# Kernel tuning notes

Hardware: AMD Instinct MI355X
Metric: run time of the kernel (lower is better)

The kernel has to match this reference:

```python
import jax, jax.numpy as jnp
import numpy as np

B, N, M = 2, 4096, 12288
K, SH, H, GK, NC, F = 64, 32, 64, 8, 200, 1


def sph_to_cart(theta, phi):
    st = jnp.sin(theta)
    return jnp.stack([st * jnp.cos(phi), st * jnp.sin(phi), jnp.cos(theta)], axis=-1)


def setup_inputs() -> dict:
    key = jax.random.key(0)
    ks = jax.random.split(key, 16)
    theta = jax.random.uniform(ks[0], (B, N)) * jnp.pi
    phi = jax.random.uniform(ks[1], (B, N)) * 2 * jnp.pi
    feat = jax.random.normal(ks[2], (B, N))
    xxx = jnp.stack([theta, phi, feat], axis=1)  # [B,3,N]
    pt = jax.random.uniform(ks[3], (M,)) * jnp.pi
    pp = jax.random.uniform(ks[4], (M,)) * 2 * jnp.pi
    pix_theta_phi = jnp.stack([pt, pp], axis=1)  # [M,2]
    s = 0.1
    return dict(
        xxx=xxx,
        pix_theta_phi=pix_theta_phi,
        att_w1=jax.random.normal(ks[5], (F + 1, SH)) * s,
        att_b1=jnp.zeros((SH,)),
        att_w2=jax.random.normal(ks[6], (SH, 1)) * s,
        att_b2=jnp.zeros((1,)),
        proj_w=jax.random.normal(ks[7], (F, H)) * s,
        proj_b=jnp.zeros((H,)),
        rel_w=jax.random.normal(ks[8], (3, H, H)) * s,
        rel_b=jnp.zeros((3, H)),
        root_w=jax.random.normal(ks[9], (3, H, H)) * s,
        out_w1=jax.random.normal(ks[10], (H, H)) * s,
        out_b1=jnp.zeros((H,)),
        out_w2=jax.random.normal(ks[11], (H, NC)) * s,
        out_b2=jnp.zeros((NC,)),
    )


def reference(xxx, pix_theta_phi, att_w1, att_b1, att_w2, att_b2, proj_w, proj_b,
              rel_w, rel_b, root_w, out_w1, out_b1, out_w2, out_b2):
    # --- sparse healpix sampler ---
    los_tp = jnp.transpose(xxx[:, :2, :], (0, 2, 1))   # [B,N,2]
    x = xxx[:, 2, :][..., None]                        # [B,N,1]
    r_los = sph_to_cart(los_tp[..., 0], los_tp[..., 1])           # [B,N,3]
    r_pix = sph_to_cart(pix_theta_phi[:, 0], pix_theta_phi[:, 1])  # [M,3]
    cos = jnp.clip(jnp.einsum('bnc,mc->bmn', r_los, r_pix), -1.0, 1.0)  # [B,M,N]
    vals, idx = jax.lax.top_k(cos, K)                  # [B,M,K]
    x_g = jax.vmap(lambda xb, ib: xb[ib])(x, idx)      # [B,M,K,F]
    d = jnp.arccos(jnp.clip(vals, -1.0, 1.0))          # [B,M,K]
    feat = jnp.concatenate([x_g, d[..., None]], axis=-1)  # [B,M,K,F+1]
    logits = jax.nn.relu(feat @ att_w1 + att_b1) @ att_w2 + att_b2  # [B,M,K,1]
    w = jax.nn.softmax(logits[..., 0], axis=-1)        # [B,M,K]
    pooled = jnp.einsum('bmk,bmkf->bmf', w, x_g)       # [B,M,F]
    # --- GNN on healpix grid ---
    h = jax.nn.relu(pooled @ proj_w + proj_b)          # [B,M,H]
    m = r_pix.shape[0]
    sq = jnp.sum(r_pix * r_pix, axis=1)
    d2 = sq[:, None] + sq[None, :] - 2.0 * (r_pix @ r_pix.T)       # [M,M]
    d2 = jnp.where(jnp.eye(m, dtype=bool), jnp.inf, d2)  # loop=False
    _, nbr = jax.lax.top_k(-d2, GK)                    # [M,GK] knn_graph
    for i in range(rel_w.shape[0]):
        agg = h[:, nbr, :].sum(axis=2)                 # sum-aggregate neighbor msgs
        h = jax.nn.relu(agg @ rel_w[i] + rel_b[i] + h @ root_w[i])
    graph_feat = h.mean(axis=1)                        # global_mean_pool -> [B,H]
    out = jax.nn.relu(graph_feat @ out_w1 + out_b1) @ out_w2 + out_b2
    return out
```

## Files before the change

### kernel.cpp

```cpp
#include <hip/hip_runtime.h>
#include <hip/hip_bf16.h>

#define B_ 2
#define N_ 4096
#define M_ 12288
#define K_ 64
#define SH_ 32
#define H_ 64
#define GK_ 8
#define NC_ 200

#define KCAP 128
#define BCAP2 48
#define SCAP 192
#define MG_ 0.01f
#define C256_ 81.48733086f

static __device__ __forceinline__ unsigned f2key(float f) {
  unsigned b = __float_as_uint(f);
  return (b & 0x80000000u) ? ~b : (b | 0x80000000u);
}
static __device__ __forceinline__ float key2f(unsigned u) {
  unsigned b = (u & 0x80000000u) ? (u & 0x7fffffffu) : ~u;
  return __uint_as_float(b);
}
static __device__ __forceinline__ unsigned long long shflxor64(unsigned long long x, int m) {
  unsigned lo = (unsigned)x, hi = (unsigned)(x >> 32);
  lo = (unsigned)__shfl_xor((int)lo, m);
  hi = (unsigned)__shfl_xor((int)hi, m);
  return ((unsigned long long)hi << 32) | lo;
}
static __device__ __forceinline__ unsigned long long kpack(float s, int j) {
  return ((unsigned long long)f2key(s) << 14) | (unsigned)(16383 - j);
}
static __device__ __forceinline__ unsigned long long spack(float c, int n) {
  return ((unsigned long long)f2key(c) << 12) | (unsigned)(4095 - n);
}
static __device__ __forceinline__ int thbkt(float th) {
  int b = (int)(th * C256_);
  return b < 0 ? 0 : (b > 255 ? 255 : b);
}
static __device__ __forceinline__ float clamp1(float x) { return fminf(1.f, fmaxf(-1.f, x)); }
static __device__ __forceinline__ float rdlane(float v, int c) {
  return __uint_as_float((unsigned)__builtin_amdgcn_readlane((int)__float_as_uint(v), c));
}

__global__ __launch_bounds__(256) void sentinel_vF(float* out, int n, float val) {
  int t = blockIdx.x * 256 + threadIdx.x;
  if (t < n) out[t] = val;
}

#define GRIDB_ 129
#define PREPN_ (M_ + B_*N_ + B_*H_)
#define PREPB_ ((PREPN_ + 255)/256)

__global__ __launch_bounds__(256) void prep_vF(
    const float* __restrict__ xxx, const float* __restrict__ pix,
    float4* __restrict__ r_pix, float4* __restrict__ r_los, float* __restrict__ gf,
    float* __restrict__ kthrG, float* __restrict__ cthrG, unsigned* __restrict__ cnt)
{
  const float PI = 3.14159265358979f;
  if ((int)blockIdx.x < GRIDB_) {
    int gid  = blockIdx.x*4 + (threadIdx.x >> 6);
    if (gid >= 514) return;
    int lane = threadIdx.x & 63;
    int tgt  = (gid >= 257) ? 1 : 0;
    int gp   = gid - tgt*257;
    float thp = (float)gp * (PI/256.f);
    float cp = cosf(thp), sp = fmaxf(sinf(thp), 1e-6f);
    float thq = ((float)lane + 0.5f) * (PI/64.f);
    float sq = sinf(thq), cq = cosf(thq);
    float rinv = 1.0f / (sq * sp);
    float At = tgt ? (2.f*PI*PI*128.f/(float)N_) : (2.f*PI*PI*48.f/(float)M_);
    float lo = 1e-3f, hi = 3.1414f;
    for (int it = 0; it < 12; ++it) {
      float al = 0.5f*(lo + hi);
      float ca = cosf(al);
      float arg = clamp1((ca - cq*cp) * rinv);
      float ax = fabsf(arg);
      float ac = sqrtf(fmaxf(0.f, 1.f - ax)) *
                 fmaf(ax, fmaf(ax, fmaf(ax, -0.0187293f, 0.0742610f), -0.2121144f), 1.5707288f);
      ac = (arg < 0.f) ? (PI - ac) : ac;
      float S = ac;
      #pragma unroll
      for (int off = 32; off; off >>= 1) S += __shfl_xor(S, off);
      float A = 2.f * S * (PI/64.f);
      if (A < At) lo = al; else hi = al;
    }
    if (lane == 0) {
      float chv = cosf(hi);
      if (tgt) cthrG[gp] = chv - 1e-5f;
      else     kthrG[gp] = 2.f*chv - 1.00002f;
    }
  } else {
    int tid = ((int)blockIdx.x - GRIDB_)*256 + threadIdx.x;
    if (tid < M_) {
      float th = pix[2*tid], ph = pix[2*tid+1];
      float st = sinf(th);
      float x = st*cosf(ph), y = st*sinf(ph), z = cosf(th);
      r_pix[tid] = make_float4(x, y, z, x*x + y*y + z*z);
      atomicAdd(&cnt[thbkt(th)], 1u);
    }
    int t2 = tid - M_;
    if (t2 >= 0 && t2 < B_*N_) {
      int b = t2 >> 12, n = t2 & (N_-1);
      const float* xb = xxx + b*3*N_;
      float th = xb[n], ph = xb[N_+n], ft = xb[2*N_+n];
      float st = sinf(th);
      r_los[t2] = make_float4(st*cosf(ph), st*sinf(ph), cosf(th), ft);
      atomicAdd(&cnt[256 + b*256 + thbkt(th)], 1u);
    }
    int t3 = tid - M_ - B_*N_;
    if (t3 >= 0 && t3 < B_*H_) gf[t3] = 0.0f;
  }
}

__global__ __launch_bounds__(256) void scan_vF(
    const unsigned* __restrict__ cnt, int* __restrict__ pstart, int* __restrict__ lstart,
    unsigned* __restrict__ pcur, unsigned* __restrict__ lcur)
{
  __shared__ unsigned buf[256];
  const int t = threadIdx.x;
  for (int arr = 0; arr < 3; ++arr) {
    unsigned v = cnt[arr*256 + t];
    buf[t] = v;
    __syncthreads();
    for (int off = 1; off < 256; off <<= 1) {
      unsigned o = (t >= off) ? buf[t - off] : 0u;
      __syncthreads();
      buf[t] += o;
      __syncthreads();
    }
    unsigned incl = buf[t], excl = incl - v;
    if (arr == 0) {
      pstart[t] = (int)excl; if (t == 255) pstart[256] = (int)incl;
      pcur[t] = excl;
    } else {
      int b = arr - 1;
      lstart[b*257 + t] = (int)excl; if (t == 255) lstart[b*257 + 256] = (int)incl;
      lcur[b*256 + t] = excl;
    }
    __syncthreads();
  }
}

__global__ __launch_bounds__(256) void scatter_vF(
    const float* __restrict__ xxx, const float* __restrict__ pix,
    const float4* __restrict__ r_pix, const float4* __restrict__ r_los,
    unsigned* __restrict__ pcur, unsigned* __restrict__ lcur,
    float4* __restrict__ spix, int* __restrict__ sjdx,
    float4* __restrict__ slos, int* __restrict__ sldx)
{
  int tid = blockIdx.x * 256 + threadIdx.x;
  if (tid < M_) {
    int bkt = thbkt(pix[2*tid]);
    unsigned pos = atomicAdd(&pcur[bkt], 1u);
    spix[pos] = r_pix[tid];
    sjdx[pos] = tid;
  } else {
    int t2 = tid - M_;
    if (t2 < B_*N_) {
      int b = t2 >> 12, n = t2 & (N_-1);
      int bkt = thbkt(xxx[b*3*N_ + n]);
      unsigned pos = atomicAdd(&lcur[b*256 + bkt], 1u);
      slos[b*N_ + pos] = r_los[t2];
      sldx[b*N_ + pos] = n;
    }
  }
}

__global__ __launch_bounds__(512) void sampler_vF(
    const float* __restrict__ pix,
    const float4* __restrict__ spix, const int* __restrict__ sjdx,
    const float4* __restrict__ slos, const int* __restrict__ sldx,
    const int* __restrict__ lstart, const float4* __restrict__ r_los,
    const float* __restrict__ cthrG,
    const float* __restrict__ aw1, const float* __restrict__ ab1,
    const float* __restrict__ aw2, const float* __restrict__ ab2,
    float* __restrict__ pooled)
{
  __shared__ unsigned long long cand[16][SCAP];
  __shared__ unsigned long long selKey[16][K_];
  __shared__ unsigned long long bndK[16][BCAP2];
  __shared__ unsigned hist[16][64];

  const int tid = threadIdx.x, wv = tid >> 6, lane = tid & 63;
  const int b  = blockIdx.y;
  const int srow0 = blockIdx.x*16 + wv*2, srow1 = srow0 + 1;
  const int r0 = wv*2, r1 = r0 + 1;
  const int m0 = sjdx[srow0], m1 = sjdx[srow1];
  const float4 p0 = spix[srow0], p1 = spix[srow1];
  const float thp0 = pix[2*m0], thp1 = pix[2*m1];
  const int g0 = thbkt(thp0), g1 = thbkt(thp1);
  const float th0 = fminf(cthrG[g0], cthrG[g0+1]);
  const float th1 = fminf(cthrG[g1], cthrG[g1+1]);
  const float inv0 = 63.999f / (1.000001f - th0);
  const float inv1 = 63.999f / (1.000001f - th1);
  const float4* sl = slos + b * N_;
  const int* sx = sldx + b * N_;
  const float4* rl = r_los + b * N_;
  const int* ls = lstart + b * 257;
  const unsigned long long ltm = (1ull << lane) - 1ull;

  int jlo, jhi;
  {
    float al0 = acosf(clamp1(th0)), al1 = acosf(clamp1(th1));
    int blo = thbkt(fminf(thp0 - al0, thp1 - al1) - MG_);
    int bhi = thbkt(fmaxf(thp0 + al0, thp1 + al1) + MG_);
    jlo = ls[blo]; jhi = ls[bhi + 1];
  }

  unsigned cnt0 = 0, cnt1 = 0;
  for (int base = jlo; base < jhi; base += 64) {
    int pos = base + lane;
    bool act = pos < jhi;
    float c0 = -2.f, c1 = -2.f; int n = 0;
    if (act) {
      float4 v = sl[pos]; n = sx[pos];
      c0 = clamp1(v.x*p0.x + v.y*p0.y + v.z*p0.z);
      c1 = clamp1(v.x*p1.x + v.y*p1.y + v.z*p1.z);
    }
    bool pr0 = c0 > th0, pr1 = c1 > th1;
    unsigned long long mk0 = __ballot(pr0);
    if (mk0) {
      unsigned off = (unsigned)__popcll(mk0 & ltm);
      if (pr0 && cnt0 + off < SCAP) cand[r0][cnt0 + off] = spack(c0, n);
      cnt0 += (unsigned)__popcll(mk0);
    }
    unsigned long long mk1 = __ballot(pr1);
    if (mk1) {
      unsigned off = (unsigned)__popcll(mk1 & ltm);
      if (pr1 && cnt1 + off < SCAP) cand[r1][cnt1 + off] = spack(c1, n);
      cnt1 += (unsigned)__popcll(mk1);
    }
  }

  for (int rr = 0; rr < 2; ++rr) {
    const int r = (rr == 0) ? r0 : r1;
    const int m = (rr == 0) ? m0 : m1;
    const float4 p = (rr == 0) ? p0 : p1;
    const float thp = (rr == 0) ? thp0 : thp1;
    const float thg = (rr == 0) ? th0 : th1;
    const float invg = (rr == 0) ? inv0 : inv1;
    unsigned cn = (rr == 0) ? cnt0 : cnt1;
    bool fin = false;

    if (cn >= (unsigned)K_ && cn <= (unsigned)SCAP) {
      hist[r][lane] = 0u;
      for (int i = lane; i < (int)cn; i += 64) {
        float c = key2f((unsigned)(cand[r][i] >> 12));
        atomicAdd(&hist[r][(int)((c - thg) * invg)], 1u);
      }
      unsigned g = hist[r][lane], s = g;
      #pragma unroll
      for (int off = 1; off < 64; off <<= 1) {
        unsigned t2 = (unsigned)__shfl_down((int)s, off);
        s += (lane + off < 64) ? t2 : 0u;
      }
      unsigned snext = s - g;
      unsigned packed = (s >= K_ && snext < K_) ? (((unsigned)(lane+1) << 16) | snext) : 0u;
      #pragma unroll
      for (int off = 32; off; off >>= 1) {
        unsigned o = (unsigned)__shfl_xor((int)packed, off);
        packed = packed > o ? packed : o;
      }
      const int t = (int)(packed >> 16) - 1;
      const unsigned chi = packed & 0xFFFFu;
      const unsigned need = K_ - chi;

      unsigned hiC = 0, bdC = 0;
      for (int i0 = 0; i0 < (int)cn; i0 += 64) {
        int i = i0 + lane;
        bool act = i < (int)cn;
        unsigned long long key = act ? cand[r][i] : 0ull;
        int bin = -1;
        if (act) bin = (int)((key2f((unsigned)(key >> 12)) - thg) * invg);
        bool pHi = act && bin > t, pBd = act && bin == t;
        unsigned long long mH = __ballot(pHi);
        unsigned offH = (unsigned)__popcll(mH & ltm);
        if (pHi && hiC + offH < K_) selKey[r][hiC + offH] = key;
        hiC += (unsigned)__popcll(mH);
        unsigned long long mB = __ballot(pBd);
        unsigned offB = (unsigned)__popcll(mB & ltm);
        if (pBd && bdC + offB < BCAP2) bndK[r][bdC + offB] = key;
        bdC += (unsigned)__popcll(mB);
      }
      if (bdC <= (unsigned)BCAP2) {
        if (lane < (int)bdC) {
          unsigned long long ki = bndK[r][lane];
          int rank = 0;
          for (int j = 0; j < (int)bdC; ++j) rank += (bndK[r][j] > ki) ? 1 : 0;
          if ((unsigned)rank < need) selKey[r][chi + rank] = ki;
        }
        fin = true;
      }
    }

    if (!fin) {
      float th = thg;
      float inv = invg;
      int wlo = jlo, whi = jhi;

      if (cn >= (unsigned)K_) {
        hist[r][lane] = 0u;
        cn = 0;
        for (int base = wlo; base < whi; base += 64) {
          int pos = base + lane;
          bool act = pos < whi;
          float c = -2.f;
          if (act) {
            float4 v = sl[pos];
            c = clamp1(v.x*p.x + v.y*p.y + v.z*p.z);
          }
          bool pr = c > th;
          if (pr) atomicAdd(&hist[r][(int)((c - th) * inv)], 1u);
          cn += (unsigned)__popcll(__ballot(pr));
        }
      }

      int tries = 0;
      while (cn < K_ && tries < 3) {
        th = 1.f - 1.6f*(1.f - th); ++tries;
        inv = 63.999f / (1.000001f - th);
        float al = acosf(clamp1(th));
        int blo = thbkt(thp - al - MG_), bhi = thbkt(thp + al + MG_);
        wlo = ls[blo]; whi = ls[bhi + 1];
        hist[r][lane] = 0u;
        cn = 0;
        for (int base = wlo; base < whi; base += 64) {
          int pos = base + lane;
          bool act = pos < whi;
          float c = -2.f;
          if (act) {
            float4 v = sl[pos];
            c = clamp1(v.x*p.x + v.y*p.y + v.z*p.z);
          }
          bool pr = c > th;
          if (pr) atomicAdd(&hist[r][(int)((c - th) * inv)], 1u);
          cn += (unsigned)__popcll(__ballot(pr));
        }
      }

      bool fin2 = false;
      if (cn >= K_) {
        unsigned g = hist[r][lane], s = g;
        #pragma unroll
        for (int off = 1; off < 64; off <<= 1) {
          unsigned t2 = (unsigned)__shfl_down((int)s, off);
          s += (lane + off < 64) ? t2 : 0u;
        }
        unsigned snext = s - g;
        unsigned packed = (s >= K_ && snext < K_) ? (((unsigned)(lane+1) << 16) | snext) : 0u;
        #pragma unroll
        for (int off = 32; off; off >>= 1) {
          unsigned o = (unsigned)__shfl_xor((int)packed, off);
          packed = packed > o ? packed : o;
        }
        const int t = (int)(packed >> 16) - 1;
        const unsigned chi = packed & 0xFFFFu;
        const unsigned need = K_ - chi;

        unsigned hiC = 0, bdC = 0;
        for (int base = wlo; base < whi; base += 64) {
          int pos = base + lane;
          bool act = pos < whi;
          float c = -2.f; int n = 0;
          if (act) {
            float4 v = sl[pos]; n = sx[pos];
            c = clamp1(v.x*p.x + v.y*p.y + v.z*p.z);
          }
          int bin = (act && c > th) ? (int)((c - th) * inv) : -1;
          bool pHi = bin > t;
          bool pBd = bin == t;
          unsigned long long mH = __ballot(pHi);
          unsigned offH = (unsigned)__popcll(mH & ltm);
          if (pHi && hiC + offH < K_) selKey[r][hiC + offH] = spack(c, n);
          hiC += (unsigned)__popcll(mH);
          unsigned long long mB = __ballot(pBd);
          unsigned offB = (unsigned)__popcll(mB & ltm);
          if (pBd && bdC + offB < BCAP2) bndK[r][bdC + offB] = spack(c, n);
          bdC += (unsigned)__popcll(mB);
        }
        if (bdC <= (unsigned)BCAP2) {
          if (lane < (int)bdC) {
            unsigned long long ki = bndK[r][lane];
            int rank = 0;
            for (int j = 0; j < (int)bdC; ++j) rank += (bndK[r][j] > ki) ? 1 : 0;
            if ((unsigned)rank < need) selKey[r][chi + rank] = ki;
          }
          fin2 = true;
        }
      }

      if (!fin2) {
        unsigned long long prev = ~0ull;
        for (int rd = 0; rd < K_; ++rd) {
          unsigned long long best = 0ull;
          for (int i = 0; i < 64; ++i) {
            int n = lane + 64*i;
            float4 v = rl[n];
            float c = clamp1(v.x*p.x + v.y*p.y + v.z*p.z);
            unsigned long long k = spack(c, n);
            if (k < prev && k > best) best = k;
          }
          #pragma unroll
          for (int off = 1; off < 64; off <<= 1) {
            unsigned long long o = shflxor64(best, off);
            best = o > best ? o : best;
          }
          if (lane == 0) selKey[r][rd] = best;
          prev = best;
        }
      }
    }

    {
      unsigned long long key = selKey[r][lane];
      int n = 4095 - (int)(key & 0xFFFull);
      float c = key2f((unsigned)(key >> 12));
      float xg = rl[n].w;
      float d  = acosf(clamp1(c));
      float acc = ab2[0];
      for (int s2 = 0; s2 < SH_; ++s2)
        acc += fmaxf(xg*aw1[s2] + d*aw1[SH_+s2] + ab1[s2], 0.f) * aw2[s2];
      float mx = acc;
      #pragma unroll
      for (int off = 32; off; off >>= 1) mx = fmaxf(mx, __shfl_xor(mx, off));
      float e = expf(acc - mx);
      float se = e, sxe = e * xg;
      #pragma unroll
      for (int off = 32; off; off >>= 1) { se += __shfl_xor(se, off); sxe += __shfl_xor(sxe, off); }
      if (lane == 0) pooled[b*M_ + m] = sxe / se;
    }
  }
}

__global__ __launch_bounds__(512) void knn_vF(
    const float* __restrict__ pix,
    const float4* __restrict__ spix, const int* __restrict__ sjdx,
    const int* __restrict__ pstart, const float4* __restrict__ r_pix,
    const float* __restrict__ kthrG, int* __restrict__ nbr)
{
  __shared__ unsigned long long cKey[16][KCAP];

  const int tid = threadIdx.x, wv = tid >> 6, lane = tid & 63;
  const int lr0 = wv*2;
  const int srow0 = blockIdx.x*16 + lr0, srow1 = srow0 + 1;
  const int i0 = sjdx[srow0], i1 = sjdx[srow1];
  const float4 p0 = spix[srow0], p1 = spix[srow1];
  const float thp0 = pix[2*i0], thp1 = pix[2*i1];
  const int g0 = thbkt(thp0), g1 = thbkt(thp1);
  const float t0 = fminf(kthrG[g0], kthrG[g0+1]);
  const float t1 = fminf(kthrG[g1], kthrG[g1+1]);
  const unsigned long long ltm = (1ull << lane) - 1ull;

  unsigned cnt0 = 0, cnt1 = 0;
  {
    float al0 = acosf(clamp1((t0 + 1.00002f)*0.5f));
    float al1 = acosf(clamp1((t1 + 1.00002f)*0.5f));
    int blo = thbkt(fminf(thp0 - al0, thp1 - al1) - MG_);
    int bhi = thbkt(fmaxf(thp0 + al0, thp1 + al1) + MG_);
    int jlo = pstart[blo], jhi = pstart[bhi + 1];
    for (int base = jlo; base < jhi; base += 64) {
      int pos = base + lane;
      bool act = pos < jhi;
      float s0 = -1e30f, s1 = -1e30f; int j = -1;
      if (act) {
        float4 v = spix[pos]; j = sjdx[pos];
        s0 = 2.f*(p0.x*v.x + p0.y*v.y + p0.z*v.z) - v.w;
        s1 = 2.f*(p1.x*v.x + p1.y*v.y + p1.z*v.z) - v.w;
      }
      bool pr0 = act && (j != i0) && (s0 > t0);
      bool pr1 = act && (j != i1) && (s1 > t1);
      unsigned long long mk0 = __ballot(pr0);
      if (mk0) {
        unsigned off = (unsigned)__popcll(mk0 & ltm);
        if (pr0 && cnt0 + off < KCAP) cKey[lr0][cnt0 + off] = kpack(s0, j);
        cnt0 += (unsigned)__popcll(mk0);
      }
      unsigned long long mk1 = __ballot(pr1);
      if (mk1) {
        unsigned off = (unsigned)__popcll(mk1 & ltm);
        if (pr1 && cnt1 + off < KCAP) cKey[lr0+1][cnt1 + off] = kpack(s1, j);
        cnt1 += (unsigned)__popcll(mk1);
      }
    }
  }

  for (int rr = 0; rr < 2; ++rr) {
    const int lr = lr0 + rr;
    const int i  = (rr == 0) ? i0 : i1;
    const float4 pi = (rr == 0) ? p0 : p1;
    const float thp = (rr == 0) ? thp0 : thp1;
    float th = (rr == 0) ? t0 : t1;
    unsigned cn = (rr == 0) ? cnt0 : cnt1;

    int tries = 0;
    while (cn < (unsigned)GK_ && tries < 3) {
      th = 1.6f*th - 0.6f; ++tries;
      float al = acosf(clamp1((th + 1.00002f)*0.5f));
      int blo = thbkt(thp - al - MG_), bhi = thbkt(thp + al + MG_);
      int jlo = pstart[blo], jhi = pstart[bhi + 1];
      cn = 0;
      for (int base = jlo; base < jhi; base += 64) {
        int pos = base + lane;
        bool act = pos < jhi;
        float s = -1e30f; int j = -1;
        if (act) {
          float4 v = spix[pos]; j = sjdx[pos];
          s = 2.f*(pi.x*v.x + pi.y*v.y + pi.z*v.z) - v.w;
        }
        bool pr = act && (j != i) && (s > th);
        unsigned long long mk = __ballot(pr);
        if (mk) {
          unsigned off = (unsigned)__popcll(mk & ltm);
          if (pr && cn + off < KCAP) cKey[lr][cn + off] = kpack(s, j);
          cn += (unsigned)__popcll(mk);
        }
      }
    }

    if (cn >= (unsigned)GK_ && cn <= (unsigned)KCAP) {
      unsigned long long pk[2];
      #pragma unroll
      for (int t2 = 0; t2 < 2; ++t2) {
        int idx = lane + 64*t2;
        pk[t2] = (idx < (int)cn) ? cKey[lr][idx] : 0ull;
      }
      for (int round = 0; round < GK_; ++round) {
        unsigned long long loc = pk[0]; int lt = 0;
        if (pk[1] > loc) { loc = pk[1]; lt = 1; }
        unsigned long long best = loc;
        #pragma unroll
        for (int off = 1; off < 64; off <<= 1) {
          unsigned long long o = shflxor64(best, off);
          best = o > best ? o : best;
        }
        if (loc == best) pk[lt] = 0ull;
        if (lane == round) nbr[i*GK_ + round] = 16383 - (int)(best & 16383ull);
      }
    } else {
      unsigned long long prev = ~0ull;
      for (int rd = 0; rd < GK_; ++rd) {
        unsigned long long best = 0ull;
        for (int j = lane; j < M_; j += 64) {
          float4 v = r_pix[j];
          float s = 2.f*(pi.x*v.x + pi.y*v.y + pi.z*v.z) - v.w;
          if (j != i) {
            unsigned long long k = kpack(s, j);
            if (k < prev && k > best) best = k;
          }
        }
        #pragma unroll
        for (int off = 1; off < 64; off <<= 1) {
          unsigned long long o = shflxor64(best, off);
          best = o > best ? o : best;
        }
        if (lane == rd) nbr[i*GK_ + rd] = 16383 - (int)(best & 16383ull);
        prev = best;
      }
    }
  }
}

__global__ __launch_bounds__(256) void gnn1f_vF(
    const float* __restrict__ pooled, float* __restrict__ hout, const int* __restrict__ nbr,
    const float* __restrict__ pw, const float* __restrict__ pb,
    const float* __restrict__ relw, const float* __restrict__ relb,
    const float* __restrict__ rootw)
{
  __shared__ float wrel[H_*H_], wroot[H_*H_];
  const int tid = threadIdx.x;
  #pragma unroll
  for (int q = 0; q < 16; ++q) {
    int idx = tid + 256*q;
    wrel[idx]  = relw[idx];
    wroot[idx] = rootw[idx];
  }
  __syncthreads();

  const int lane = tid & 63;
  const int wave = tid >> 6;
  const int b = blockIdx.y;
  const int m0 = blockIdx.x * 16 + wave * 4;
  const float* pldb = pooled + (size_t)b * M_;
  const float pwl = pw[lane], pbl = pb[lane], rbl = relb[lane];

  float h[4], agg[4], acc[4];
  #pragma unroll
  for (int t = 0; t < 4; ++t) {
    int m = m0 + t;
    float ps = pldb[m];
    h[t] = fmaxf(ps*pwl + pbl, 0.f);
    float a = 0.f;
    #pragma unroll
    for (int k = 0; k < GK_; ++k) {
      int nb = nbr[m*GK_ + k];
      nb = nb < 0 ? 0 : (nb >= M_ ? M_-1 : nb);
      float pn = pldb[nb];
      a += fmaxf(pn*pwl + pbl, 0.f);
    }
    agg[t] = a;
    acc[t] = rbl;
  }
  #pragma unroll
  for (int c = 0; c < H_; ++c) {
    float wr = wrel[c*H_ + lane], wo = wroot[c*H_ + lane];
    #pragma unroll
    for (int t = 0; t < 4; ++t)
      acc[t] += rdlane(agg[t], c) * wr + rdlane(h[t], c) * wo;
  }
  #pragma unroll
  for (int t = 0; t < 4; ++t)
    hout[((size_t)b*M_ + m0 + t)*H_ + lane] = fmaxf(acc[t], 0.f);
}

__global__ __launch_bounds__(256) void gnn_vF(
    const float* __restrict__ hin, float* __restrict__ hout, const int* __restrict__ nbr,
    const float* __restrict__ relw, const float* __restrict__ relb,
    const float* __restrict__ rootw)
{
  __shared__ float wrel[H_*H_], wroot[H_*H_];
  const int tid = threadIdx.x;
  #pragma unroll
  for (int q = 0; q < 16; ++q) {
    int idx = tid + 256*q;
    wrel[idx]  = relw[idx];
    wroot[idx] = rootw[idx];
  }
  __syncthreads();

  const int lane = tid & 63;
  const int wave = tid >> 6;
  const int b = blockIdx.y;
  const int m0 = blockIdx.x * 16 + wave * 4;
  const float* hb = hin + (size_t)b * M_ * H_;
  const float rbl = relb[lane];

  float h[4], agg[4], acc[4];
  #pragma unroll
  for (int t = 0; t < 4; ++t) {
    int m = m0 + t;
    h[t] = hb[m*H_ + lane];
    float a = 0.f;
    #pragma unroll
    for (int k = 0; k < GK_; ++k) {
      int nb = nbr[m*GK_ + k];
      nb = nb < 0 ? 0 : (nb >= M_ ? M_-1 : nb);
      a += hb[nb*H_ + lane];
    }
    agg[t] = a;
    acc[t] = rbl;
  }
  #pragma unroll
  for (int c = 0; c < H_; ++c) {
    float wr = wrel[c*H_ + lane], wo = wroot[c*H_ + lane];
    #pragma unroll
    for (int t = 0; t < 4; ++t)
      acc[t] += rdlane(agg[t], c) * wr + rdlane(h[t], c) * wo;
  }
  #pragma unroll
  for (int t = 0; t < 4; ++t)
    hout[((size_t)b*M_ + m0 + t)*H_ + lane] = fmaxf(acc[t], 0.f);
}

__global__ __launch_bounds__(256) void gnn3r_vF(
    const float* __restrict__ hin, float* __restrict__ gf, const int* __restrict__ nbr,
    const float* __restrict__ relw, const float* __restrict__ relb,
    const float* __restrict__ rootw)
{
  __shared__ float wrel[H_*H_], wroot[H_*H_];
  __shared__ float gacc[H_];
  const int tid = threadIdx.x;
  #pragma unroll
  for (int q = 0; q < 16; ++q) {
    int idx = tid + 256*q;
    wrel[idx]  = relw[idx];
    wroot[idx] = rootw[idx];
  }
  if (tid < H_) gacc[tid] = 0.f;
  __syncthreads();

  const int lane = tid & 63;
  const int wave = tid >> 6;
  const int b = blockIdx.y;
  const int m0 = blockIdx.x * 16 + wave * 4;
  const float* hb = hin + (size_t)b * M_ * H_;
  const float rbl = relb[lane];

  float h[4], agg[4], acc[4];
  #pragma unroll
  for (int t = 0; t < 4; ++t) {
    int m = m0 + t;
    h[t] = hb[m*H_ + lane];
    float a = 0.f;
    #pragma unroll
    for (int k = 0; k < GK_; ++k) {
      int nb = nbr[m*GK_ + k];
      nb = nb < 0 ? 0 : (nb >= M_ ? M_-1 : nb);
      a += hb[nb*H_ + lane];
    }
    agg[t] = a;
    acc[t] = rbl;
  }
  #pragma unroll
  for (int c = 0; c < H_; ++c) {
    float wr = wrel[c*H_ + lane], wo = wroot[c*H_ + lane];
    #pragma unroll
    for (int t = 0; t < 4; ++t)
      acc[t] += rdlane(agg[t], c) * wr + rdlane(h[t], c) * wo;
  }
  float ps = fmaxf(acc[0], 0.f) + fmaxf(acc[1], 0.f) + fmaxf(acc[2], 0.f) + fmaxf(acc[3], 0.f);
  atomicAdd(&gacc[lane], ps);
  __syncthreads();
  if (tid < H_) atomicAdd(&gf[b*H_ + tid], gacc[tid]);
}

__global__ __launch_bounds__(256) void head_vF(
    const float* __restrict__ gf, const float* __restrict__ w1,
    const float* __restrict__ b1, const float* __restrict__ w2,
    const float* __restrict__ b2, float* __restrict__ out)
{
  __shared__ float gfm[B_][H_], hid[B_][H_];
  const int tid = threadIdx.x;
  if (tid < B_*H_) gfm[tid >> 6][tid & 63] = gf[tid] * (1.f / (float)M_);
  __syncthreads();
  if (tid < B_*H_) {
    int b = tid >> 6, j = tid & 63;
    float acc = b1[j];
    for (int c = 0; c < H_; ++c) acc += gfm[b][c] * w1[c*H_ + j];
    hid[b][j] = fmaxf(acc, 0.f);
  }
  __syncthreads();
  for (int t = tid; t < B_*NC_; t += 256) {
    int b = t / NC_, o = t - b*NC_;
    float acc = b2[o];
    for (int j = 0; j < H_; ++j) acc += hid[b][j] * w2[j*NC_ + o];
    out[t] = acc;
  }
}

extern "C" void kernel_launch(void* const* d_in, const int* in_sizes, int n_in,
                              void* d_out, int out_size, void* d_ws, size_t ws_size,
                              hipStream_t stream)
{
  float* out = (float*)d_out;

  const size_t need = (size_t)M_*16 + (size_t)B_*N_*16 + (size_t)B_*M_*4
                    + (size_t)M_*GK_*4 + 2*(size_t)B_*M_*H_*4 + (size_t)B_*H_*4;
  bool ok_ws = ws_size >= need;
  bool ok_in = (n_in == 15) && (out_size == B_*NC_)
            && in_sizes[0] == B_*3*N_ && in_sizes[1] == M_*2
            && in_sizes[2] == 2*SH_ && in_sizes[5] == 1
            && in_sizes[8] == 3*H_*H_ && in_sizes[13] == H_*NC_;
  if (!ok_ws || !ok_in) {
    sentinel_vF<<<(out_size + 255)/256, 256, 0, stream>>>(out, out_size, ok_in ? 42.f : 43.f);
    return;
  }

  const float* xxx    = (const float*)d_in[0];
  const float* pix    = (const float*)d_in[1];
  const float* att_w1 = (const float*)d_in[2];
  const float* att_b1 = (const float*)d_in[3];
  const float* att_w2 = (const float*)d_in[4];
  const float* att_b2 = (const float*)d_in[5];
  const float* proj_w = (const float*)d_in[6];
  const float* proj_b = (const float*)d_in[7];
  const float* rel_w  = (const float*)d_in[8];
  const float* rel_b  = (const float*)d_in[9];
  const float* root_w = (const float*)d_in[10];
  const float* out_w1 = (const float*)d_in[11];
  const float* out_b1 = (const float*)d_in[12];
  const float* out_w2 = (const float*)d_in[13];
  const float* out_b2 = (const float*)d_in[14];

  char* w = (char*)d_ws;
  float4* r_pix = (float4*)w;  w += (size_t)M_ * 16;
  float4* r_los = (float4*)w;  w += (size_t)B_ * N_ * 16;
  float*  pooled = (float*)w;  w += (size_t)B_ * M_ * 4;
  int*    nbr = (int*)w;       w += (size_t)M_ * GK_ * 4;
  float*  h0 = (float*)w;      w += (size_t)B_ * M_ * H_ * 4;
  float*  h1 = (float*)w;      w += (size_t)B_ * M_ * H_ * 4;
  float*  gf = (float*)w;      w += (size_t)B_ * H_ * 4;

  float*  kthrG = h0;
  float*  cthrG = h0 + 512;
  float4* spix = (float4*)(h0 + 2*M_);
  int*    sjdx = (int*)(h0 + 6*M_);
  float4* slos = (float4*)(h0 + 7*M_);
  int*    sldx = (int*)(h0 + 7*M_ + 4*B_*N_);
  unsigned* cnt = (unsigned*)(h0 + 7*M_ + 5*B_*N_);
  int*    pstart = (int*)(cnt + 768);
  int*    lstart = pstart + 257;
  unsigned* pcur = (unsigned*)(lstart + 514);
  unsigned* lcur = pcur + 256;

  hipMemsetAsync(cnt, 0, 768*sizeof(unsigned), stream);
  prep_vF<<<GRIDB_ + PREPB_, 256, 0, stream>>>(xxx, pix, r_pix, r_los, gf, kthrG, cthrG, cnt);
  scan_vF<<<1, 256, 0, stream>>>(cnt, pstart, lstart, pcur, lcur);
  scatter_vF<<<(M_ + B_*N_ + 255)/256, 256, 0, stream>>>(xxx, pix, r_pix, r_los, pcur, lcur,
                                                         spix, sjdx, slos, sldx);
  sampler_vF<<<dim3(M_/16, B_), 512, 0, stream>>>(pix, spix, sjdx, slos, sldx, lstart, r_los,
                                                  cthrG, att_w1, att_b1, att_w2, att_b2, pooled);
  knn_vF<<<M_/16, 512, 0, stream>>>(pix, spix, sjdx, pstart, r_pix, kthrG, nbr);
  gnn1f_vF<<<dim3(M_/16, B_), 256, 0, stream>>>(pooled, h1, nbr, proj_w, proj_b,
                                                rel_w + 0*H_*H_, rel_b + 0*H_, root_w + 0*H_*H_);
  gnn_vF<<<dim3(M_/16, B_), 256, 0, stream>>>(h1, h0, nbr, rel_w + 1*H_*H_, rel_b + 1*H_, root_w + 1*H_*H_);
  gnn3r_vF<<<dim3(M_/16, B_), 256, 0, stream>>>(h0, gf, nbr, rel_w + 2*H_*H_, rel_b + 2*H_, root_w + 2*H_*H_);
  head_vF<<<1, 256, 0, stream>>>(gf, out_w1, out_b1, out_w2, out_b2, out);
}
```

Before: 239.2 us.

## Process four query rows per wave in sampler and kNN, tighten candidate thresholds

The sampler and kNN kernels now have each wavefront handle four sorted pixel rows instead of two. Each loaded line-of-sight or pixel vector is reused across four dot products, and the grid is halved. The angular threshold targets are lowered (96 instead of 128 candidates, 40 instead of 48) and the candidate buffer is shrunk to 128, so fewer candidates are gathered and more shared memory fits. The trade-offs are a wider per-wave window, since the union of four rows' ranges is scanned, and a higher chance of falling into the slow fallback paths when fewer than K candidates pass.

Result: slower. 267.6 us (+11.9%).

```diff
diff --git a/kernel.cpp b/kernel.cpp
--- a/kernel.cpp
+++ b/kernel.cpp
@@ -12,7 +12,7 @@
 
 #define KCAP 128
 #define BCAP2 48
-#define SCAP 192
+#define SCAP 128
 #define MG_ 0.01f
 #define C256_ 81.48733086f
 
@@ -45,7 +45,7 @@
   return __uint_as_float((unsigned)__builtin_amdgcn_readlane((int)__float_as_uint(v), c));
 }
 
-__global__ __launch_bounds__(256) void sentinel_vF(float* out, int n, float val) {
+__global__ __launch_bounds__(256) void sentinel_vI(float* out, int n, float val) {
   int t = blockIdx.x * 256 + threadIdx.x;
   if (t < n) out[t] = val;
 }
@@ -54,7 +54,7 @@
 #define PREPN_ (M_ + B_*N_ + B_*H_)
 #define PREPB_ ((PREPN_ + 255)/256)
 
-__global__ __launch_bounds__(256) void prep_vF(
+__global__ __launch_bounds__(256) void prep_vI(
     const float* __restrict__ xxx, const float* __restrict__ pix,
     float4* __restrict__ r_pix, float4* __restrict__ r_los, float* __restrict__ gf,
     float* __restrict__ kthrG, float* __restrict__ cthrG, unsigned* __restrict__ cnt)
@@ -71,7 +71,7 @@
     float thq = ((float)lane + 0.5f) * (PI/64.f);
     float sq = sinf(thq), cq = cosf(thq);
     float rinv = 1.0f / (sq * sp);
-    float At = tgt ? (2.f*PI*PI*128.f/(float)N_) : (2.f*PI*PI*48.f/(float)M_);
+    float At = tgt ? (2.f*PI*PI*96.f/(float)N_) : (2.f*PI*PI*40.f/(float)M_);
     float lo = 1e-3f, hi = 3.1414f;
     for (int it = 0; it < 12; ++it) {
       float al = 0.5f*(lo + hi);
@@ -115,7 +115,7 @@
   }
 }
 
-__global__ __launch_bounds__(256) void scan_vF(
+__global__ __launch_bounds__(256) void scan_vI(
     const unsigned* __restrict__ cnt, int* __restrict__ pstart, int* __restrict__ lstart,
     unsigned* __restrict__ pcur, unsigned* __restrict__ lcur)
 {
@@ -144,7 +144,7 @@
   }
 }
 
-__global__ __launch_bounds__(256) void scatter_vF(
+__global__ __launch_bounds__(256) void scatter_vI(
     const float* __restrict__ xxx, const float* __restrict__ pix,
     const float4* __restrict__ r_pix, const float4* __restrict__ r_los,
     unsigned* __restrict__ pcur, unsigned* __restrict__ lcur,
@@ -169,7 +169,7 @@
   }
 }
 
-__global__ __launch_bounds__(512) void sampler_vF(
+__global__ __launch_bounds__(512) void sampler_vI(
     const float* __restrict__ pix,
     const float4* __restrict__ spix, const int* __restrict__ sjdx,
     const float4* __restrict__ slos, const int* __restrict__ sldx,
@@ -179,79 +179,83 @@
     const float* __restrict__ aw2, const float* __restrict__ ab2,
     float* __restrict__ pooled)
 {
-  __shared__ unsigned long long cand[16][SCAP];
-  __shared__ unsigned long long selKey[16][K_];
-  __shared__ unsigned long long bndK[16][BCAP2];
-  __shared__ unsigned hist[16][64];
+  __shared__ unsigned long long cand[32][SCAP];
+  __shared__ unsigned long long selKey[32][K_];
+  __shared__ unsigned long long bndK[8][BCAP2];
+  __shared__ unsigned hist[8][64];
 
   const int tid = threadIdx.x, wv = tid >> 6, lane = tid & 63;
   const int b  = blockIdx.y;
-  const int srow0 = blockIdx.x*16 + wv*2, srow1 = srow0 + 1;
-  const int r0 = wv*2, r1 = r0 + 1;
-  const int m0 = sjdx[srow0], m1 = sjdx[srow1];
-  const float4 p0 = spix[srow0], p1 = spix[srow1];
-  const float thp0 = pix[2*m0], thp1 = pix[2*m1];
-  const int g0 = thbkt(thp0), g1 = thbkt(thp1);
-  const float th0 = fminf(cthrG[g0], cthrG[g0+1]);
-  const float th1 = fminf(cthrG[g1], cthrG[g1+1]);
-  const float inv0 = 63.999f / (1.000001f - th0);
-  const float inv1 = 63.999f / (1.000001f - th1);
+  const int srow0 = blockIdx.x*32 + wv*4;
+  const int r0 = wv*4;
   const float4* sl = slos + b * N_;
   const int* sx = sldx + b * N_;
   const float4* rl = r_los + b * N_;
   const int* ls = lstart + b * 257;
   const unsigned long long ltm = (1ull << lane) - 1ull;
 
+  float4 p[4]; float thp[4], thr[4], invr[4]; int mI[4];
+  #pragma unroll
+  for (int rr = 0; rr < 4; ++rr) {
+    int sr = srow0 + rr;
+    mI[rr] = sjdx[sr];
+    p[rr] = spix[sr];
+    thp[rr] = pix[2*mI[rr]];
+    int g = thbkt(thp[rr]);
+    thr[rr] = fminf(cthrG[g], cthrG[g+1]);
+    invr[rr] = 63.999f / (1.000001f - thr[rr]);
+  }
+
   int jlo, jhi;
   {
-    float al0 = acosf(clamp1(th0)), al1 = acosf(clamp1(th1));
-    int blo = thbkt(fminf(thp0 - al0, thp1 - al1) - MG_);
-    int bhi = thbkt(fmaxf(thp0 + al0, thp1 + al1) + MG_);
-    jlo = ls[blo]; jhi = ls[bhi + 1];
-  }
-
-  unsigned cnt0 = 0, cnt1 = 0;
+    float wl = 1e9f, wh = -1e9f;
+    #pragma unroll
+    for (int rr = 0; rr < 4; ++rr) {
+      float al = acosf(clamp1(thr[rr]));
+      wl = fminf(wl, thp[rr] - al);
+      wh = fmaxf(wh, thp[rr] + al);
+    }
+    jlo = ls[thbkt(wl - MG_)];
+    jhi = ls[thbkt(wh + MG_) + 1];
+  }
+
+  unsigned cnt[4] = {0u, 0u, 0u, 0u};
   for (int base = jlo; base < jhi; base += 64) {
     int pos = base + lane;
     bool act = pos < jhi;
-    float c0 = -2.f, c1 = -2.f; int n = 0;
-    if (act) {
-      float4 v = sl[pos]; n = sx[pos];
-      c0 = clamp1(v.x*p0.x + v.y*p0.y + v.z*p0.z);
-      c1 = clamp1(v.x*p1.x + v.y*p1.y + v.z*p1.z);
-    }
-    bool pr0 = c0 > th0, pr1 = c1 > th1;
-    unsigned long long mk0 = __ballot(pr0);
-    if (mk0) {
-      unsigned off = (unsigned)__popcll(mk0 & ltm);
-      if (pr0 && cnt0 + off < SCAP) cand[r0][cnt0 + off] = spack(c0, n);
-      cnt0 += (unsigned)__popcll(mk0);
-    }
-    unsigned long long mk1 = __ballot(pr1);
-    if (mk1) {
-      unsigned off = (unsigned)__popcll(mk1 & ltm);
-      if (pr1 && cnt1 + off < SCAP) cand[r1][cnt1 + off] = spack(c1, n);
-      cnt1 += (unsigned)__popcll(mk1);
-    }
-  }
-
-  for (int rr = 0; rr < 2; ++rr) {
-    const int r = (rr == 0) ? r0 : r1;
-    const int m = (rr == 0) ? m0 : m1;
-    const float4 p = (rr == 0) ? p0 : p1;
-    const float thp = (rr == 0) ? thp0 : thp1;
-    const float thg = (rr == 0) ? th0 : th1;
-    const float invg = (rr == 0) ? inv0 : inv1;
-    unsigned cn = (rr == 0) ? cnt0 : cnt1;
+    float4 v = make_float4(0.f, 0.f, 0.f, 0.f); int n = 0;
+    if (act) { v = sl[pos]; n = sx[pos]; }
+    #pragma unroll
+    for (int rr = 0; rr < 4; ++rr) {
+      float c = clamp1(v.x*p[rr].x + v.y*p[rr].y + v.z*p[rr].z);
+      bool pr = act && (c > thr[rr]);
+      unsigned long long mk = __ballot(pr);
+      if (mk) {
+        unsigned off = (unsigned)__popcll(mk & ltm);
+        if (pr && cnt[rr] + off < SCAP) cand[r0+rr][cnt[rr] + off] = spack(c, n);
+        cnt[rr] += (unsigned)__popcll(mk);
+      }
+    }
+  }
+
+  #pragma unroll
+  for (int rr = 0; rr < 4; ++rr) {
+    const int r = r0 + rr;
+    const int m = mI[rr];
+    const float4 pq = p[rr];
+    const float thpq = thp[rr];
+    const float thg = thr[rr];
+    const float invg = invr[rr];
+    unsigned cn = cnt[rr];
     bool fin = false;
 
     if (cn >= (unsigned)K_ && cn <= (unsigned)SCAP) {
-      hist[r][lane] = 0u;
+      hist[wv][lane] = 0u;
       for (int i = lane; i < (int)cn; i += 64) {
         float c = key2f((unsigned)(cand[r][i] >> 12));
-        atomicAdd(&hist[r][(int)((c - thg) * invg)], 1u);
-      }
-      unsigned g = hist[r][lane], s = g;
+        atomicAdd(&hist[wv][(int)((c - thg) * invg)], 1u);
+      }
+      unsigned g = hist[wv][lane], s = g;
       #pragma unroll
       for (int off = 1; off < 64; off <<= 1) {
         unsigned t2 = (unsigned)__shfl_down((int)s, off);
@@ -282,14 +286,14 @@
         hiC += (unsigned)__popcll(mH);
         unsigned long long mB = __ballot(pBd);
         unsigned offB = (unsigned)__popcll(mB & ltm);
-        if (pBd && bdC + offB < BCAP2) bndK[r][bdC + offB] = key;
+        if (pBd && bdC + offB < BCAP2) bndK[wv][bdC + offB] = key;
         bdC += (unsigned)__popcll(mB);
       }
       if (bdC <= (unsigned)BCAP2) {
         if (lane < (int)bdC) {
-          unsigned long long ki = bndK[r][lane];
+          unsigned long long ki = bndK[wv][lane];
           int rank = 0;
-          for (int j = 0; j < (int)bdC; ++j) rank += (bndK[r][j] > ki) ? 1 : 0;
+          for (int j = 0; j < (int)bdC; ++j) rank += (bndK[wv][j] > ki) ? 1 : 0;
           if ((unsigned)rank < need) selKey[r][chi + rank] = ki;
         }
         fin = true;
@@ -302,7 +306,7 @@
       int wlo = jlo, whi = jhi;
 
       if (cn >= (unsigned)K_) {
-        hist[r][lane] = 0u;
+        hist[wv][lane] = 0u;
         cn = 0;
         for (int base = wlo; base < whi; base += 64) {
           int pos = base + lane;
@@ -310,10 +314,10 @@
           float c = -2.f;
           if (act) {
             float4 v = sl[pos];
-            c = clamp1(v.x*p.x + v.y*p.y + v.z*p.z);
+            c = clamp1(v.x*pq.x + v.y*pq.y + v.z*pq.z);
           }
           bool pr = c > th;
-          if (pr) atomicAdd(&hist[r][(int)((c - th) * inv)], 1u);
+          if (pr) atomicAdd(&hist[wv][(int)((c - th) * inv)], 1u);
           cn += (unsigned)__popcll(__ballot(pr));
         }
       }
@@ -323,9 +327,9 @@
         th = 1.f - 1.6f*(1.f - th); ++tries;
         inv = 63.999f / (1.000001f - th);
         float al = acosf(clamp1(th));
-        int blo = thbkt(thp - al - MG_), bhi = thbkt(thp + al + MG_);
+        int blo = thbkt(thpq - al - MG_), bhi = thbkt(thpq + al + MG_);
         wlo = ls[blo]; whi = ls[bhi + 1];
-        hist[r][lane] = 0u;
+        hist[wv][lane] = 0u;
         cn = 0;
         for (int base = wlo; base < whi; base += 64) {
           int pos = base + lane;
@@ -333,17 +337,17 @@
           float c = -2.f;
           if (act) {
             float4 v = sl[pos];
-            c = clamp1(v.x*p.x + v.y*p.y + v.z*p.z);
+            c = clamp1(v.x*pq.x + v.y*pq.y + v.z*pq.z);
           }
           bool pr = c > th;
-          if (pr) atomicAdd(&hist[r][(int)((c - th) * inv)], 1u);
+          if (pr) atomicAdd(&hist[wv][(int)((c - th) * inv)], 1u);
           cn += (unsigned)__popcll(__ballot(pr));
         }
       }
 
       bool fin2 = false;
       if (cn >= K_) {
-        unsigned g = hist[r][lane], s = g;
+        unsigned g = hist[wv][lane], s = g;
         #pragma unroll
         for (int off = 1; off < 64; off <<= 1) {
           unsigned t2 = (unsigned)__shfl_down((int)s, off);
@@ -367,7 +371,7 @@
           float c = -2.f; int n = 0;
           if (act) {
             float4 v = sl[pos]; n = sx[pos];
-            c = clamp1(v.x*p.x + v.y*p.y + v.z*p.z);
+            c = clamp1(v.x*pq.x + v.y*pq.y + v.z*pq.z);
           }
           int bin = (act && c > th) ? (int)((c - th) * inv) : -1;
           bool pHi = bin > t;
@@ -378,14 +382,14 @@
           hiC += (unsigned)__popcll(mH);
           unsigned long long mB = __ballot(pBd);
           unsigned offB = (unsigned)__popcll(mB & ltm);
-          if (pBd && bdC + offB < BCAP2) bndK[r][bdC + offB] = spack(c, n);
+          if (pBd && bdC + offB < BCAP2) bndK[wv][bdC + offB] = spack(c, n);
           bdC += (unsigned)__popcll(mB);
         }
         if (bdC <= (unsigned)BCAP2) {
           if (lane < (int)bdC) {
-            unsigned long long ki = bndK[r][lane];
+            unsigned long long ki = bndK[wv][lane];
             int rank = 0;
-            for (int j = 0; j < (int)bdC; ++j) rank += (bndK[r][j] > ki) ? 1 : 0;
+            for (int j = 0; j < (int)bdC; ++j) rank += (bndK[wv][j] > ki) ? 1 : 0;
             if ((unsigned)rank < need) selKey[r][chi + rank] = ki;
           }
           fin2 = true;
@@ -399,7 +403,7 @@
           for (int i = 0; i < 64; ++i) {
             int n = lane + 64*i;
             float4 v = rl[n];
-            float c = clamp1(v.x*p.x + v.y*p.y + v.z*p.z);
+            float c = clamp1(v.x*pq.x + v.y*pq.y + v.z*pq.z);
             unsigned long long k = spack(c, n);
             if (k < prev && k > best) best = k;
           }
@@ -435,71 +439,73 @@
   }
 }
 
-__global__ __launch_bounds__(512) void knn_vF(
+__global__ __launch_bounds__(512) void knn_vI(
     const float* __restrict__ pix,
     const float4* __restrict__ spix, const int* __restrict__ sjdx,
     const int* __restrict__ pstart, const float4* __restrict__ r_pix,
     const float* __restrict__ kthrG, int* __restrict__ nbr)
 {
-  __shared__ unsigned long long cKey[16][KCAP];
+  __shared__ unsigned long long cKey[32][KCAP];
 
   const int tid = threadIdx.x, wv = tid >> 6, lane = tid & 63;
-  const int lr0 = wv*2;
-  const int srow0 = blockIdx.x*16 + lr0, srow1 = srow0 + 1;
-  const int i0 = sjdx[srow0], i1 = sjdx[srow1];
-  const float4 p0 = spix[srow0], p1 = spix[srow1];
-  const float thp0 = pix[2*i0], thp1 = pix[2*i1];
-  const int g0 = thbkt(thp0), g1 = thbkt(thp1);
-  const float t0 = fminf(kthrG[g0], kthrG[g0+1]);
-  const float t1 = fminf(kthrG[g1], kthrG[g1+1]);
+  const int lr0 = wv*4;
+  const int srow0 = blockIdx.x*32 + lr0;
   const unsigned long long ltm = (1ull << lane) - 1ull;
 
-  unsigned cnt0 = 0, cnt1 = 0;
+  float4 p[4]; float thp[4], thr[4]; int iI[4];
+  #pragma unroll
+  for (int rr = 0; rr < 4; ++rr) {
+    int sr = srow0 + rr;
+    iI[rr] = sjdx[sr];
+    p[rr] = spix[sr];
+    thp[rr] = pix[2*iI[rr]];
+    int g = thbkt(thp[rr]);
+    thr[rr] = fminf(kthrG[g], kthrG[g+1]);
+  }
+
+  unsigned cnt[4] = {0u, 0u, 0u, 0u};
   {
-    float al0 = acosf(clamp1((t0 + 1.00002f)*0.5f));
-    float al1 = acosf(clamp1((t1 + 1.00002f)*0.5f));
-    int blo = thbkt(fminf(thp0 - al0, thp1 - al1) - MG_);
-    int bhi = thbkt(fmaxf(thp0 + al0, thp1 + al1) + MG_);
-    int jlo = pstart[blo], jhi = pstart[bhi + 1];
+    float wl = 1e9f, wh = -1e9f;
+    #pragma unroll
+    for (int rr = 0; rr < 4; ++rr) {
+      float al = acosf(clamp1((thr[rr] + 1.00002f)*0.5f));
+      wl = fminf(wl, thp[rr] - al);
+      wh = fmaxf(wh, thp[rr] + al);
+    }
+    int jlo = pstart[thbkt(wl - MG_)], jhi = pstart[thbkt(wh + MG_) + 1];
     for (int base = jlo; base < jhi; base += 64) {
       int pos = base + lane;
       bool act = pos < jhi;
-      float s0 = -1e30f, s1 = -1e30f; int j = -1;
-      if (act) {
-        float4 v = spix[pos]; j = sjdx[pos];
-        s0 = 2.f*(p0.x*v.x + p0.y*v.y + p0.z*v.z) - v.w;
-        s1 = 2.f*(p1.x*v.x + p1.y*v.y + p1.z*v.z) - v.w;
-      }
-      bool pr0 = act && (j != i0) && (s0 > t0);
-      bool pr1 = act && (j != i1) && (s1 > t1);
-      unsigned long long mk0 = __ballot(pr0);
-      if (mk0) {
-        unsigned off = (unsigned)__popcll(mk0 & ltm);
-        if (pr0 && cnt0 + off < KCAP) cKey[lr0][cnt0 + off] = kpack(s0, j);
-        cnt0 += (unsigned)__popcll(mk0);
-      }
-      unsigned long long mk1 = __ballot(pr1);
-      if (mk1) {
-        unsigned off = (unsigned)__popcll(mk1 & ltm);
-        if (pr1 && cnt1 + off < KCAP) cKey[lr0+1][cnt1 + off] = kpack(s1, j);
-        cnt1 += (unsigned)__popcll(mk1);
-      }
-    }
-  }
-
-  for (int rr = 0; rr < 2; ++rr) {
+      float4 v = make_float4(0.f, 0.f, 0.f, 0.f); int j = -1;
+      if (act) { v = spix[pos]; j = sjdx[pos]; }
+      #pragma unroll
+      for (int rr = 0; rr < 4; ++rr) {
+        float s = 2.f*(p[rr].x*v.x + p[rr].y*v.y + p[rr].z*v.z) - v.w;
+        bool pr = act && (j != iI[rr]) && (s > thr[rr]);
+        unsigned long long mk = __ballot(pr);
+        if (mk) {
+          unsigned off = (unsigned)__popcll(mk & ltm);
+          if (pr && cnt[rr] + off < KCAP) cKey[lr0+rr][cnt[rr] + off] = kpack(s, j);
+          cnt[rr] += (unsigned)__popcll(mk);
+        }
+      }
+    }
+  }
+
+  #pragma unroll
+  for (int rr = 0; rr < 4; ++rr) {
     const int lr = lr0 + rr;
-    const int i  = (rr == 0) ? i0 : i1;
-    const float4 pi = (rr == 0) ? p0 : p1;
-    const float thp = (rr == 0) ? thp0 : thp1;
-    float th = (rr == 0) ? t0 : t1;
-    unsigned cn = (rr == 0) ? cnt0 : cnt1;
+    const int i  = iI[rr];
+    const float4 pi = p[rr];
+    const float thpq = thp[rr];
+    float th = thr[rr];
+    unsigned cn = cnt[rr];
 
     int tries = 0;
     while (cn < (unsigned)GK_ && tries < 3) {
       th = 1.6f*th - 0.6f; ++tries;
       float al = acosf(clamp1((th + 1.00002f)*0.5f));
-      int blo = thbkt(thp - al - MG_), bhi = thbkt(thp + al + MG_);
+      int blo = thbkt(thpq - al - MG_), bhi = thbkt(thpq + al + MG_);
       int jlo = pstart[blo], jhi = pstart[bhi + 1];
       cn = 0;
       for (int base = jlo; base < jhi; base += 64) {
@@ -563,7 +569,7 @@
   }
 }
 
-__global__ __launch_bounds__(256) void gnn1f_vF(
+__global__ __launch_bounds__(256) void gnn1f_vI(
     const float* __restrict__ pooled, float* __restrict__ hout, const int* __restrict__ nbr,
     const float* __restrict__ pw, const float* __restrict__ pb,
     const float* __restrict__ relw, const float* __restrict__ relb,
@@ -615,7 +621,7 @@
     hout[((size_t)b*M_ + m0 + t)*H_ + lane] = fmaxf(acc[t], 0.f);
 }
 
-__global__ __launch_bounds__(256) void gnn_vF(
+__global__ __launch_bounds__(256) void gnn_vI(
     const float* __restrict__ hin, float* __restrict__ hout, const int* __restrict__ nbr,
     const float* __restrict__ relw, const float* __restrict__ relb,
     const float* __restrict__ rootw)
@@ -664,7 +670,7 @@
     hout[((size_t)b*M_ + m0 + t)*H_ + lane] = fmaxf(acc[t], 0.f);
 }
 
-__global__ __launch_bounds__(256) void gnn3r_vF(
+__global__ __launch_bounds__(256) void gnn3r_vI(
     const float* __restrict__ hin, float* __restrict__ gf, const int* __restrict__ nbr,
     const float* __restrict__ relw, const float* __restrict__ relb,
     const float* __restrict__ rootw)
@@ -716,7 +722,7 @@
   if (tid < H_) atomicAdd(&gf[b*H_ + tid], gacc[tid]);
 }
 
-__global__ __launch_bounds__(256) void head_vF(
+__global__ __launch_bounds__(256) void head_vI(
     const float* __restrict__ gf, const float* __restrict__ w1,
     const float* __restrict__ b1, const float* __restrict__ w2,
     const float* __restrict__ b2, float* __restrict__ out)
@@ -754,7 +760,7 @@
             && in_sizes[2] == 2*SH_ && in_sizes[5] == 1
             && in_sizes[8] == 3*H_*H_ && in_sizes[13] == H_*NC_;
   if (!ok_ws || !ok_in) {
-    sentinel_vF<<<(out_size + 255)/256, 256, 0, stream>>>(out, out_size, ok_in ? 42.f : 43.f);
+    sentinel_vI<<<(out_size + 255)/256, 256, 0, stream>>>(out, out_size, ok_in ? 42.f : 43.f);
     return;
   }
 
@@ -796,16 +802,16 @@
   unsigned* lcur = pcur + 256;
 
   hipMemsetAsync(cnt, 0, 768*sizeof(unsigned), stream);
-  prep_vF<<<GRIDB_ + PREPB_, 256, 0, stream>>>(xxx, pix, r_pix, r_los, gf, kthrG, cthrG, cnt);
-  scan_vF<<<1, 256, 0, stream>>>(cnt, pstart, lstart, pcur, lcur);
-  scatter_vF<<<(M_ + B_*N_ + 255)/256, 256, 0, stream>>>(xxx, pix, r_pix, r_los, pcur, lcur,
+  prep_vI<<<GRIDB_ + PREPB_, 256, 0, stream>>>(xxx, pix, r_pix, r_los, gf, kthrG, cthrG, cnt);
+  scan_vI<<<1, 256, 0, stream>>>(cnt, pstart, lstart, pcur, lcur);
+  scatter_vI<<<(M_ + B_*N_ + 255)/256, 256, 0, stream>>>(xxx, pix, r_pix, r_los, pcur, lcur,
                                                          spix, sjdx, slos, sldx);
-  sampler_vF<<<dim3(M_/16, B_), 512, 0, stream>>>(pix, spix, sjdx, slos, sldx, lstart, r_los,
+  sampler_vI<<<dim3(M_/32, B_), 512, 0, stream>>>(pix, spix, sjdx, slos, sldx, lstart, r_los,
                                                   cthrG, att_w1, att_b1, att_w2, att_b2, pooled);
-  knn_vF<<<M_/16, 512, 0, stream>>>(pix, spix, sjdx, pstart, r_pix, kthrG, nbr);
-  gnn1f_vF<<<dim3(M_/16, B_), 256, 0, stream>>>(pooled, h1, nbr, proj_w, proj_b,
+  knn_vI<<<M_/32, 512, 0, stream>>>(pix, spix, sjdx, pstart, r_pix, kthrG, nbr);
+  gnn1f_vI<<<dim3(M_/16, B_), 256, 0, stream>>>(pooled, h1, nbr, proj_w, proj_b,
                                                 rel_w + 0*H_*H_, rel_b + 0*H_, root_w + 0*H_*H_);
-  gnn_vF<<<dim3(M_/16, B_), 256, 0, stream>>>(h1, h0, nbr, rel_w + 1*H_*H_, rel_b + 1*H_, root_w + 1*H_*H_);
-  gnn3r_vF<<<dim3(M_/16, B_), 256, 0, stream>>>(h0, gf, nbr, rel_w + 2*H_*H_, rel_b + 2*H_, root_w + 2*H_*H_);
-  head_vF<<<1, 256, 0, stream>>>(gf, out_w1, out_b1, out_w2, out_b2, out);
-}
+  gnn_vI<<<dim3(M_/16, B_), 256, 0, stream>>>(h1, h0, nbr, rel_w + 1*H_*H_, rel_b + 1*H_, root_w + 1*H_*H_);
+  gnn3r_vI<<<dim3(M_/16, B_), 256, 0, stream>>>(h0, gf, nbr, rel_w + 2*H_*H_, rel_b + 2*H_, root_w + 2*H_*H_);
+  head_vI<<<1, 256, 0, stream>>>(gf, out_w1, out_b1, out_w2, out_b2, out);
+}
```
